# Kernel tuning notes

Measured on AMD Instinct MI355X. Metric: run time of the kernel, lower is better.

Reference implementation:

```python
import jax, jax.numpy as jnp
import numpy as np
import math

RIEMANN_ZEROS_IM = (14.134725142, 21.022039639, 25.01085758, 30.424876126, 32.935061588,
    37.586178159, 40.918719012, 43.327073281, 48.005150881, 49.773832478, 52.970321478,
    56.446247697, 59.347044003, 60.831778525, 65.112544048, 67.079810529, 69.546401711,
    72.067157674, 75.704690699, 77.144840069, 79.33737502, 82.910380854, 84.735492981,
    87.425274613, 88.809111208, 92.491899271, 94.651344041, 95.870634228, 98.831194218,
    101.317851006, 103.72553804, 105.446623052)

D_MODEL = 1024
N_HEADS = 16
D_HEAD = D_MODEL // N_HEADS  # 64
N_PAIRS = D_HEAD // 2        # 32

# normalized inverse frequencies: gamma_n / gamma_1, inverted
_gamma = np.asarray(RIEMANN_ZEROS_IM[:N_PAIRS], dtype=np.float32)
INV_FREQ = jnp.asarray(1.0 / (_gamma / _gamma[0]))  # [n_pairs]


def _rotate(x, cos, sin):
    # x: [b,h,n,d_head]; cos/sin: [1,h,n,n_pairs]; interleaved pair rotation
    x1 = x[..., 0::2]
    x2 = x[..., 1::2]
    rx1 = x1 * cos - x2 * sin
    rx2 = x1 * sin + x2 * cos
    return jnp.stack([rx1, rx2], axis=-1).reshape(x.shape)


def setup_inputs() -> dict:
    key = jax.random.key(0)
    k1, k2, k3 = jax.random.split(key, 3)
    b, n = 4, 2048
    x = jax.random.normal(k1, (b, n, D_MODEL), dtype=jnp.float32)
    # torch Linear(d, 3d, bias=False): y = x @ W.T; we store W.T directly
    w_qkv = jax.random.normal(k2, (D_MODEL, 3 * D_MODEL), dtype=jnp.float32) / math.sqrt(D_MODEL)
    w_o = jax.random.normal(k3, (D_MODEL, D_MODEL), dtype=jnp.float32) / math.sqrt(D_MODEL)
    log_scale = jnp.zeros((N_HEADS,), dtype=jnp.float32)
    return {"x": x, "w_qkv": w_qkv, "w_o": w_o, "log_scale": log_scale}


def reference(x, w_qkv, w_o, log_scale):
    b, n, d = x.shape
    qkv = (x @ w_qkv).reshape(b, n, 3, N_HEADS, D_HEAD)
    q, k, v = qkv[:, :, 0], qkv[:, :, 1], qkv[:, :, 2]  # [b,n,h,dh]
    q = q.transpose(0, 2, 1, 3)  # [b,h,n,dh]
    k = k.transpose(0, 2, 1, 3)
    v = v.transpose(0, 2, 1, 3)

    scale = jnp.exp(log_scale)  # [h]
    pos = jnp.arange(n, dtype=jnp.float32)
    # theta: [1,h,n,n_pairs]
    theta = pos[None, None, :, None] * INV_FREQ[None, None, None, :] * scale[None, :, None, None]
    cos, sin = jnp.cos(theta), jnp.sin(theta)
    q = _rotate(q, cos, sin)
    k = _rotate(k, cos, sin)

    scores = jnp.einsum('bhqd,bhkd->bhqk', q, k) / math.sqrt(D_HEAD)
    causal = jnp.tril(jnp.ones((n, n), dtype=bool))
    scores = jnp.where(causal[None, None], scores, -jnp.inf)
    attn = jax.nn.softmax(scores, axis=-1)
    out = jnp.einsum('bhqk,bhkd->bhqd', attn, v)
    out = out.transpose(0, 2, 1, 3).reshape(b, n, d)
    return out @ w_o
```

## Files before the change

kernel.cpp:

```cpp
#include <hip/hip_runtime.h>
#include <hip/hip_bf16.h>

#define B_ 4
#define N_ 2048
#define DM 1024
#define NH 16
#define DH 64

typedef __attribute__((ext_vector_type(8))) __bf16 bf16x8;
typedef __attribute__((ext_vector_type(4))) float f32x4;
typedef __attribute__((ext_vector_type(4))) float float4v;
typedef __attribute__((ext_vector_type(4))) unsigned int uint4v;
typedef __attribute__((ext_vector_type(2))) unsigned int uint2v;
typedef __attribute__((ext_vector_type(4))) unsigned short ushort4v;

__device__ __forceinline__ float bf2f(unsigned short h) {
  union { unsigned int u; float f; } v; v.u = ((unsigned int)h) << 16; return v.f;
}
__device__ __forceinline__ unsigned short f2bf(float f) {
  __bf16 h = (__bf16)f;
  return __builtin_bit_cast(unsigned short, h);
}
__device__ __forceinline__ f32x4 mfma16(bf16x8 a, bf16x8 b, f32x4 c) {
  return __builtin_amdgcn_mfma_f32_16x16x32_bf16(a, b, c, 0, 0, 0);
}
__device__ __forceinline__ void gload_lds16(const void* g, void* l) {
  __builtin_amdgcn_global_load_lds(
      (const __attribute__((address_space(1))) unsigned int*)g,
      (__attribute__((address_space(3))) unsigned int*)l, 16, 0, 0);
}
__device__ __forceinline__ float fexp2(float x) {
  return __builtin_amdgcn_exp2f(x);
}

__constant__ float GAMMA_C[32] = {
  14.134725142f, 21.022039639f, 25.01085758f, 30.424876126f,
  32.935061588f, 37.586178159f, 40.918719012f, 43.327073281f,
  48.005150881f, 49.773832478f, 52.970321478f, 56.446247697f,
  59.347044003f, 60.831778525f, 65.112544048f, 67.079810529f,
  69.546401711f, 72.067157674f, 75.704690699f, 77.144840069f,
  79.33737502f,  82.910380854f, 84.735492981f, 87.425274613f,
  88.809111208f, 92.491899271f, 94.651344041f, 95.870634228f,
  98.831194218f, 101.317851006f, 103.72553804f, 105.446623052f
};

__global__ __launch_bounds__(256) void cast_f32_bf16(
    const float* __restrict__ in, unsigned short* __restrict__ out, int n4) {
  int i = blockIdx.x * 256 + threadIdx.x;
  if (i >= n4) return;
  float4v v = *(const float4v*)&in[(size_t)i * 4];
  ushort4v o;
  o[0] = f2bf(v[0]); o[1] = f2bf(v[1]); o[2] = f2bf(v[2]); o[3] = f2bf(v[3]);
  *(ushort4v*)&out[(size_t)i * 4] = o;
}

__global__ __launch_bounds__(256) void tcast(
    const float* __restrict__ in, unsigned short* __restrict__ out, int K, int N) {
  __shared__ float t[32][33];
  int n0 = blockIdx.x * 32, k0 = blockIdx.y * 32;
  int tx = threadIdx.x, ty = threadIdx.y;
#pragma unroll
  for (int j = 0; j < 4; ++j)
    t[ty + j * 8][tx] = in[(size_t)(k0 + ty + j * 8) * N + n0 + tx];
  __syncthreads();
#pragma unroll
  for (int j = 0; j < 4; ++j)
    out[(size_t)(n0 + ty + j * 8) * K + k0 + tx] = f2bf(t[tx][ty + j * 8]);
}

template <int OUTF32>
__global__ __launch_bounds__(256) void gemm_bt(
    const unsigned short* __restrict__ A, const unsigned short* __restrict__ BT,
    void* __restrict__ C, int M, int N, int K) {
  __shared__ unsigned short As[128 * 32];
  __shared__ unsigned short Bs[128 * 32];
  int tid = threadIdx.x;
  int lane = tid & 63, wid = tid >> 6;
  int wr = wid >> 1, wc = wid & 1;
  int lr = lane & 15, lg = lane >> 4;
  int bm = blockIdx.y * 128, bn = blockIdx.x * 128;
  int srow = lane >> 2, sch = lane & 3;
  f32x4 acc[4][4];
#pragma unroll
  for (int m = 0; m < 4; ++m)
#pragma unroll
    for (int n = 0; n < 4; ++n) acc[m][n] = (f32x4){0.f, 0.f, 0.f, 0.f};

  for (int k0 = 0; k0 < K; k0 += 32) {
    __syncthreads();
#pragma unroll
    for (int it = 0; it < 2; ++it) {
      int rbase = wid * 16 + it * 64;
      gload_lds16(&A[(size_t)(bm + rbase + srow) * K + k0 + sch * 8],
                  &As[rbase * 32]);
      gload_lds16(&BT[(size_t)(bn + rbase + srow) * K + k0 + sch * 8],
                  &Bs[rbase * 32]);
    }
    __syncthreads();
    bf16x8 af[4], bfr[4];
#pragma unroll
    for (int m = 0; m < 4; ++m)
      af[m] = *(const bf16x8*)&As[(wr * 64 + m * 16 + lr) * 32 + lg * 8];
#pragma unroll
    for (int n = 0; n < 4; ++n)
      bfr[n] = *(const bf16x8*)&Bs[(wc * 64 + n * 16 + lr) * 32 + lg * 8];
    __builtin_amdgcn_s_setprio(1);
#pragma unroll
    for (int m = 0; m < 4; ++m)
#pragma unroll
      for (int n = 0; n < 4; ++n)
        acc[m][n] = mfma16(af[m], bfr[n], acc[m][n]);
    __builtin_amdgcn_s_setprio(0);
  }
#pragma unroll
  for (int m = 0; m < 4; ++m)
#pragma unroll
    for (int n = 0; n < 4; ++n) {
      int row = bm + wr * 64 + m * 16 + lg * 4;
      int col = bn + wc * 64 + n * 16 + lr;
#pragma unroll
      for (int r = 0; r < 4; ++r) {
        if (OUTF32)
          ((float*)C)[(size_t)(row + r) * N + col] = acc[m][n][r];
        else
          ((unsigned short*)C)[(size_t)(row + r) * N + col] = f2bf(acc[m][n][r]);
      }
    }
}

__global__ __launch_bounds__(256) void rope_split(
    const unsigned short* __restrict__ qkv, const float* __restrict__ log_scale,
    unsigned short* __restrict__ Qr, unsigned short* __restrict__ Kr,
    unsigned short* __restrict__ Vr) {
  const float SC = 0.125f * 1.44269504089f;
  int t = blockIdx.x * 256 + threadIdx.x;
  int p = t & 31, h = (t >> 5) & 15, n = (t >> 9) & 2047, b = t >> 20;
  float invf = GAMMA_C[0] / GAMMA_C[p];
  float scale = __expf(log_scale[h]);
  float theta = ((float)n * invf) * scale;
  float sn, cs;
  sincosf(theta, &sn, &cs);
  size_t base = (size_t)(b * N_ + n) * (3 * DM) + h * DH + 2 * p;
  unsigned int qu = *(const unsigned int*)&qkv[base];
  unsigned int ku = *(const unsigned int*)&qkv[base + DM];
  unsigned int vu = *(const unsigned int*)&qkv[base + 2 * DM];
  float q1 = bf2f(qu & 0xffffu), q2 = bf2f(qu >> 16);
  float k1 = bf2f(ku & 0xffffu), k2 = bf2f(ku >> 16);
  unsigned int rq = (unsigned int)f2bf((q1 * cs - q2 * sn) * SC) |
                    ((unsigned int)f2bf((q1 * sn + q2 * cs) * SC) << 16);
  unsigned int rk = (unsigned int)f2bf(k1 * cs - k2 * sn) |
                    ((unsigned int)f2bf(k1 * sn + k2 * cs) << 16);
  size_t ob = (size_t)((b * NH + h) * N_ + n) * DH + 2 * p;
  *(unsigned int*)&Qr[ob] = rq;
  *(unsigned int*)&Kr[ob] = rk;
  *(unsigned int*)&Vr[ob] = vu;
}

__global__ __launch_bounds__(256) void attn_fwd(
    const unsigned short* __restrict__ Q, const unsigned short* __restrict__ K,
    const unsigned short* __restrict__ V, unsigned short* __restrict__ AO) {
  int orig = blockIdx.x;
  int wg = (orig & 7) * 128 + (orig >> 3);
  int i = wg & 15;
  int qt = ((wg >> 5) & 1) ? (15 - i) : i;
  int bh = wg >> 4;
  int b = bh >> 4, h = bh & 15;
  int q0 = qt * 128;
  int tid = threadIdx.x;
  int lane = tid & 63, w = tid >> 6;
  int lr = lane & 15, lg = lane >> 4;

  const unsigned short* Qh = Q + (size_t)bh * N_ * DH;
  const unsigned short* Kh = K + (size_t)bh * N_ * DH;
  const unsigned short* Vh = V + (size_t)bh * N_ * DH;

  __shared__ unsigned short Ks[64 * 64];
  __shared__ unsigned short Vt[64 * 64];
  __shared__ unsigned int PsU[4][32][32];

  bf16x8 qf[2][2];
#pragma unroll
  for (int m = 0; m < 2; ++m)
#pragma unroll
    for (int dh = 0; dh < 2; ++dh)
      qf[m][dh] = *(const bf16x8*)
          &Qh[(size_t)(q0 + w * 32 + m * 16 + lr) * DH + dh * 32 + lg * 8];

  f32x4 oacc[2][4];
#pragma unroll
  for (int m = 0; m < 2; ++m)
#pragma unroll
    for (int nb = 0; nb < 4; ++nb) oacc[m][nb] = (f32x4){0.f, 0.f, 0.f, 0.f};
  float mst[2] = {-1e30f, -1e30f};
  float lst[2] = {0.f, 0.f};

  int wkend = q0 + w * 32 + 31;
  int ksup = q0 + 128;
  int vch = tid & 7, vk = tid >> 3;
  int swz = 4 * (lr & 7);

  for (int k0 = 0; k0 < ksup; k0 += 64) {
    __syncthreads();
#pragma unroll
    for (int it = 0; it < 2; ++it) {
      int rbase = w * 8 + it * 32;
      int row = rbase + (lane >> 3);
      int sk = ((row & 7) ^ (row >> 3)) & 7;
      int ch = lane & 7;
      gload_lds16(&Kh[(size_t)(k0 + row) * DH + ((ch ^ sk) * 8)],
                  &Ks[rbase * 64]);
    }
#pragma unroll
    for (int it = 0; it < 2; ++it) {
      int k = vk + it * 32;
      uint4v vv = *(const uint4v*)&Vh[(size_t)(k0 + k) * DH + vch * 8];
      const unsigned short* pv = (const unsigned short*)&vv;
#pragma unroll
      for (int j = 0; j < 8; ++j) {
        int d = vch * 8 + j;
        int sv = (j ^ vch) & 7;
        Vt[d * 64 + (k ^ (sv << 3))] = pv[j];
      }
    }
    __syncthreads();
    if (k0 > wkend) continue;

    f32x4 s[2][4];
    __builtin_amdgcn_s_setprio(1);
#pragma unroll
    for (int nb = 0; nb < 4; ++nb) {
      int key = nb * 16 + lr;
      int sk = ((key & 7) ^ (key >> 3)) & 7;
      bf16x8 kf0 = *(const bf16x8*)&Ks[key * 64 + ((lg ^ sk) * 8)];
      bf16x8 kf1 = *(const bf16x8*)&Ks[key * 64 + (((4 + lg) ^ sk) * 8)];
#pragma unroll
      for (int m = 0; m < 2; ++m) {
        f32x4 z = (f32x4){0.f, 0.f, 0.f, 0.f};
        z = mfma16(kf0, qf[m][0], z);
        z = mfma16(kf1, qf[m][1], z);
        s[m][nb] = z;
      }
    }
    __builtin_amdgcn_s_setprio(0);

    float mx[2];
#pragma unroll
    for (int m = 0; m < 2; ++m) {
      int qm = q0 + w * 32 + m * 16;
      if (k0 + 63 > qm) {
        int q = qm + lr;
#pragma unroll
        for (int nb = 0; nb < 4; ++nb)
#pragma unroll
          for (int r = 0; r < 4; ++r)
            if (k0 + nb * 16 + lg * 4 + r > q) s[m][nb][r] = -1e30f;
      }
      float mx0 = fmaxf(fmaxf(s[m][0][0], s[m][0][1]),
                        fmaxf(s[m][0][2], s[m][0][3]));
      float mx1 = fmaxf(fmaxf(s[m][1][0], s[m][1][1]),
                        fmaxf(s[m][1][2], s[m][1][3]));
      float mx2 = fmaxf(fmaxf(s[m][2][0], s[m][2][1]),
                        fmaxf(s[m][2][2], s[m][2][3]));
      float mx3 = fmaxf(fmaxf(s[m][3][0], s[m][3][1]),
                        fmaxf(s[m][3][2], s[m][3][3]));
      float m01 = fmaxf(fmaxf(mx0, mx1), fmaxf(mx2, mx3));
      m01 = fmaxf(m01, __shfl_xor(m01, 16, 64));
      m01 = fmaxf(m01, __shfl_xor(m01, 32, 64));
      mx[m] = m01;
    }

    if (__any((mx[0] > mst[0] + 8.f) || (mx[1] > mst[1] + 8.f))) {
      float scs[2];
#pragma unroll
      for (int m = 0; m < 2; ++m) {
        float mnew = fmaxf(mst[m], mx[m]);
        float sc = fexp2(mst[m] - mnew);
        mst[m] = mnew;
        lst[m] *= sc;
        scs[m] = sc;
      }
#pragma unroll
      for (int m = 0; m < 2; ++m)
#pragma unroll
        for (int r = 0; r < 4; ++r) {
          float scr = __shfl(scs[m], lg * 4 + r, 64);
#pragma unroll
          for (int nb = 0; nb < 4; ++nb) oacc[m][nb][r] *= scr;
        }
    }

#pragma unroll
    for (int m = 0; m < 2; ++m) {
      float ps = 0.f;
      unsigned int pw[8];
#pragma unroll
      for (int nb = 0; nb < 4; ++nb)
#pragma unroll
        for (int rp = 0; rp < 2; ++rp) {
          float p0 = fexp2(s[m][nb][2 * rp] - mst[m]);
          float p1 = fexp2(s[m][nb][2 * rp + 1] - mst[m]);
          ps += p0 + p1;
          pw[nb * 2 + rp] =
              (unsigned int)f2bf(p0) | ((unsigned int)f2bf(p1) << 16);
        }
#pragma unroll
      for (int nb = 0; nb < 4; ++nb) {
        int c0 = (nb * 8 + lg * 2) ^ swz;
        *(uint2v*)&PsU[w][m * 16 + lr][c0] = (uint2v){pw[nb * 2], pw[nb * 2 + 1]};
      }
      ps += __shfl_xor(ps, 16, 64);
      ps += __shfl_xor(ps, 32, 64);
      lst[m] += ps;
    }
    asm volatile("s_waitcnt lgkmcnt(0)" ::: "memory");
    __builtin_amdgcn_sched_barrier(0);

    __builtin_amdgcn_s_setprio(1);
#pragma unroll
    for (int kh = 0; kh < 2; ++kh) {
      bf16x8 pf0 = *(const bf16x8*)&PsU[w][lr][(kh * 16 + lg * 4) ^ swz];
      bf16x8 pf1 = *(const bf16x8*)&PsU[w][16 + lr][(kh * 16 + lg * 4) ^ swz];
#pragma unroll
      for (int nb = 0; nb < 4; ++nb) {
        int d = nb * 16 + lr;
        int sv2 = ((d & 7) ^ (d >> 3)) & 7;
        bf16x8 vf = *(const bf16x8*)
            &Vt[d * 64 + ((kh * 32 + lg * 8) ^ (sv2 << 3))];
        oacc[0][nb] = mfma16(pf0, vf, oacc[0][nb]);
        oacc[1][nb] = mfma16(pf1, vf, oacc[1][nb]);
      }
    }
    __builtin_amdgcn_s_setprio(0);
  }

#pragma unroll
  for (int m = 0; m < 2; ++m) {
    float inv = 1.0f / lst[m];
#pragma unroll
    for (int r = 0; r < 4; ++r) {
      float invr = __shfl(inv, lg * 4 + r, 64);
      int q = q0 + w * 32 + m * 16 + lg * 4 + r;
#pragma unroll
      for (int nb = 0; nb < 4; ++nb) {
        float o = oacc[m][nb][r] * invr;
        AO[(size_t)(b * N_ + q) * DM + h * DH + nb * 16 + lr] = f2bf(o);
      }
    }
  }
}

extern "C" void kernel_launch(void* const* d_in, const int* in_sizes, int n_in,
                              void* d_out, int out_size, void* d_ws, size_t ws_size,
                              hipStream_t stream) {
  const float* x = (const float*)d_in[0];
  const float* w_qkv = (const float*)d_in[1];
  const float* w_o = (const float*)d_in[2];
  const float* log_scale = (const float*)d_in[3];
  float* out = (float*)d_out;

  char* ws = (char*)d_ws;
  unsigned short* xb  = (unsigned short*)(ws);
  unsigned short* ao  = xb;
  unsigned short* wqT = (unsigned short*)(ws + (16u << 20));
  unsigned short* woT = (unsigned short*)(ws + (22u << 20));
  unsigned short* qkv = (unsigned short*)(ws + (24u << 20));
  unsigned short* Qr  = (unsigned short*)(ws + (72u << 20));
  unsigned short* Kr  = (unsigned short*)(ws + (88u << 20));
  unsigned short* Vr  = (unsigned short*)(ws + (104u << 20));

  cast_f32_bf16<<<8192, 256, 0, stream>>>(x, xb, (B_ * N_ * DM) / 4);
  dim3 tb(32, 8);
  tcast<<<dim3(3 * DM / 32, DM / 32), tb, 0, stream>>>(w_qkv, wqT, DM, 3 * DM);
  tcast<<<dim3(DM / 32, DM / 32), tb, 0, stream>>>(w_o, woT, DM, DM);
  gemm_bt<0><<<dim3(3 * DM / 128, (B_ * N_) / 128), 256, 0, stream>>>(
      xb, wqT, qkv, B_ * N_, 3 * DM, DM);
  rope_split<<<(B_ * N_ * NH * 32) / 256, 256, 0, stream>>>(
      qkv, log_scale, Qr, Kr, Vr);
  attn_fwd<<<B_ * NH * (N_ / 128), 256, 0, stream>>>(Qr, Kr, Vr, ao);
  gemm_bt<1><<<dim3(DM / 128, (B_ * N_) / 128), 256, 0, stream>>>(
      ao, woT, out, B_ * N_, DM, DM);
}
```

Before: 246.0 us.

## Fuse RoPE and Q/K head split into QKV GEMM epilogue, read V in place

Removes the separate rope_split kernel. The QKV GEMM epilogue now applies the rotary rotation, using a lane shuffle to fetch the pair partner, and writes Q and K directly in head-major layout, while V stays in the interleaved qkv buffer. Attention reads V with a strided row pitch instead of from a contiguous per-head buffer. This saves one kernel launch and a full read and write pass over the QKV tensor, at the cost of per-element sincos in the GEMM epilogue and less coalesced V loads.

```diff
diff --git a/kernel.cpp b/kernel.cpp
--- a/kernel.cpp
+++ b/kernel.cpp
@@ -128,37 +128,99 @@
     }
 }
 
-__global__ __launch_bounds__(256) void rope_split(
-    const unsigned short* __restrict__ qkv, const float* __restrict__ log_scale,
-    unsigned short* __restrict__ Qr, unsigned short* __restrict__ Kr,
-    unsigned short* __restrict__ Vr) {
-  const float SC = 0.125f * 1.44269504089f;
-  int t = blockIdx.x * 256 + threadIdx.x;
-  int p = t & 31, h = (t >> 5) & 15, n = (t >> 9) & 2047, b = t >> 20;
-  float invf = GAMMA_C[0] / GAMMA_C[p];
-  float scale = __expf(log_scale[h]);
-  float theta = ((float)n * invf) * scale;
-  float sn, cs;
-  sincosf(theta, &sn, &cs);
-  size_t base = (size_t)(b * N_ + n) * (3 * DM) + h * DH + 2 * p;
-  unsigned int qu = *(const unsigned int*)&qkv[base];
-  unsigned int ku = *(const unsigned int*)&qkv[base + DM];
-  unsigned int vu = *(const unsigned int*)&qkv[base + 2 * DM];
-  float q1 = bf2f(qu & 0xffffu), q2 = bf2f(qu >> 16);
-  float k1 = bf2f(ku & 0xffffu), k2 = bf2f(ku >> 16);
-  unsigned int rq = (unsigned int)f2bf((q1 * cs - q2 * sn) * SC) |
-                    ((unsigned int)f2bf((q1 * sn + q2 * cs) * SC) << 16);
-  unsigned int rk = (unsigned int)f2bf(k1 * cs - k2 * sn) |
-                    ((unsigned int)f2bf(k1 * sn + k2 * cs) << 16);
-  size_t ob = (size_t)((b * NH + h) * N_ + n) * DH + 2 * p;
-  *(unsigned int*)&Qr[ob] = rq;
-  *(unsigned int*)&Kr[ob] = rk;
-  *(unsigned int*)&Vr[ob] = vu;
+__global__ __launch_bounds__(256) void gemm_qkv_rope(
+    const unsigned short* __restrict__ A, const unsigned short* __restrict__ BT,
+    unsigned short* __restrict__ qkvV, unsigned short* __restrict__ Qr,
+    unsigned short* __restrict__ Kr, const float* __restrict__ log_scale,
+    int M, int N, int K) {
+  __shared__ unsigned short As[128 * 32];
+  __shared__ unsigned short Bs[128 * 32];
+  int tid = threadIdx.x;
+  int lane = tid & 63, wid = tid >> 6;
+  int wr = wid >> 1, wc = wid & 1;
+  int lr = lane & 15, lg = lane >> 4;
+  int bm = blockIdx.y * 128, bn = blockIdx.x * 128;
+  int srow = lane >> 2, sch = lane & 3;
+  f32x4 acc[4][4];
+#pragma unroll
+  for (int m = 0; m < 4; ++m)
+#pragma unroll
+    for (int n = 0; n < 4; ++n) acc[m][n] = (f32x4){0.f, 0.f, 0.f, 0.f};
+
+  for (int k0 = 0; k0 < K; k0 += 32) {
+    __syncthreads();
+#pragma unroll
+    for (int it = 0; it < 2; ++it) {
+      int rbase = wid * 16 + it * 64;
+      gload_lds16(&A[(size_t)(bm + rbase + srow) * K + k0 + sch * 8],
+                  &As[rbase * 32]);
+      gload_lds16(&BT[(size_t)(bn + rbase + srow) * K + k0 + sch * 8],
+                  &Bs[rbase * 32]);
+    }
+    __syncthreads();
+    bf16x8 af[4], bfr[4];
+#pragma unroll
+    for (int m = 0; m < 4; ++m)
+      af[m] = *(const bf16x8*)&As[(wr * 64 + m * 16 + lr) * 32 + lg * 8];
+#pragma unroll
+    for (int n = 0; n < 4; ++n)
+      bfr[n] = *(const bf16x8*)&Bs[(wc * 64 + n * 16 + lr) * 32 + lg * 8];
+    __builtin_amdgcn_s_setprio(1);
+#pragma unroll
+    for (int m = 0; m < 4; ++m)
+#pragma unroll
+      for (int n = 0; n < 4; ++n)
+        acc[m][n] = mfma16(af[m], bfr[n], acc[m][n]);
+    __builtin_amdgcn_s_setprio(0);
+  }
+
+  int region = bn >> 10;
+  if (region == 2) {
+#pragma unroll
+    for (int m = 0; m < 4; ++m)
+#pragma unroll
+      for (int n = 0; n < 4; ++n) {
+        int row = bm + wr * 64 + m * 16 + lg * 4;
+        int col = bn + wc * 64 + n * 16 + lr;
+#pragma unroll
+        for (int r = 0; r < 4; ++r)
+          qkvV[(size_t)(row + r) * N + col] = f2bf(acc[m][n][r]);
+      }
+  } else {
+    const float SCq = 0.125f * 1.44269504089f;
+    unsigned short* dst = region ? Kr : Qr;
+#pragma unroll
+    for (int n = 0; n < 4; ++n) {
+      int col = bn + wc * 64 + n * 16 + lr;
+      int h = (col >> 6) & 15;
+      int p = (col & 63) >> 1;
+      int d = col & 63;
+      bool odd = (col & 1) != 0;
+      float w0 = (GAMMA_C[0] / GAMMA_C[p]) * __expf(log_scale[h]);
+#pragma unroll
+      for (int m = 0; m < 4; ++m) {
+#pragma unroll
+        for (int r = 0; r < 4; ++r) {
+          int row = bm + wr * 64 + m * 16 + lg * 4 + r;
+          int npos = row & (N_ - 1);
+          int bb = row >> 11;
+          float th = (float)npos * w0;
+          float sn, cs;
+          sincosf(th, &sn, &cs);
+          float v = acc[m][n][r];
+          float pv = __shfl_xor(v, 1, 64);
+          float out = odd ? (pv * sn + v * cs) : (v * cs - pv * sn);
+          if (region == 0) out *= SCq;
+          dst[((size_t)(bb * NH + h) * N_ + npos) * DH + d] = f2bf(out);
+        }
+      }
+    }
+  }
 }
 
 __global__ __launch_bounds__(256) void attn_fwd(
     const unsigned short* __restrict__ Q, const unsigned short* __restrict__ K,
-    const unsigned short* __restrict__ V, unsigned short* __restrict__ AO) {
+    const unsigned short* __restrict__ qkv, unsigned short* __restrict__ AO) {
   int orig = blockIdx.x;
   int wg = (orig & 7) * 128 + (orig >> 3);
   int i = wg & 15;
@@ -172,7 +234,7 @@
 
   const unsigned short* Qh = Q + (size_t)bh * N_ * DH;
   const unsigned short* Kh = K + (size_t)bh * N_ * DH;
-  const unsigned short* Vh = V + (size_t)bh * N_ * DH;
+  const unsigned short* Vq = qkv + (size_t)b * N_ * (3 * DM) + 2 * DM + h * DH;
 
   __shared__ unsigned short Ks[64 * 64];
   __shared__ unsigned short Vt[64 * 64];
@@ -213,7 +275,7 @@
 #pragma unroll
     for (int it = 0; it < 2; ++it) {
       int k = vk + it * 32;
-      uint4v vv = *(const uint4v*)&Vh[(size_t)(k0 + k) * DH + vch * 8];
+      uint4v vv = *(const uint4v*)&Vq[(size_t)(k0 + k) * (3 * DM) + vch * 8];
       const unsigned short* pv = (const unsigned short*)&vv;
 #pragma unroll
       for (int j = 0; j < 8; ++j) {
@@ -366,17 +428,14 @@
   unsigned short* qkv = (unsigned short*)(ws + (24u << 20));
   unsigned short* Qr  = (unsigned short*)(ws + (72u << 20));
   unsigned short* Kr  = (unsigned short*)(ws + (88u << 20));
-  unsigned short* Vr  = (unsigned short*)(ws + (104u << 20));
 
   cast_f32_bf16<<<8192, 256, 0, stream>>>(x, xb, (B_ * N_ * DM) / 4);
   dim3 tb(32, 8);
   tcast<<<dim3(3 * DM / 32, DM / 32), tb, 0, stream>>>(w_qkv, wqT, DM, 3 * DM);
   tcast<<<dim3(DM / 32, DM / 32), tb, 0, stream>>>(w_o, woT, DM, DM);
-  gemm_bt<0><<<dim3(3 * DM / 128, (B_ * N_) / 128), 256, 0, stream>>>(
-      xb, wqT, qkv, B_ * N_, 3 * DM, DM);
-  rope_split<<<(B_ * N_ * NH * 32) / 256, 256, 0, stream>>>(
-      qkv, log_scale, Qr, Kr, Vr);
-  attn_fwd<<<B_ * NH * (N_ / 128), 256, 0, stream>>>(Qr, Kr, Vr, ao);
+  gemm_qkv_rope<<<dim3(3 * DM / 128, (B_ * N_) / 128), 256, 0, stream>>>(
+      xb, wqT, qkv, Qr, Kr, log_scale, B_ * N_, 3 * DM, DM);
+  attn_fwd<<<B_ * NH * (N_ / 128), 256, 0, stream>>>(Qr, Kr, qkv, ao);
   gemm_bt<1><<<dim3(DM / 128, (B_ * N_) / 128), 256, 0, stream>>>(
       ao, woT, out, B_ * N_, DM, DM);
 }
```

After: 695.4 us. 183% more time.
